# Kernel tuning notes

Measured on AMD Instinct MI355X. Metric: run time of the kernel, lower is better.

The kernel has to match this reference:

```python
import jax, jax.numpy as jnp
import numpy as np

F = 128          # num_features
NRBF = 20        # num_rbf_features
N_NODES = 25000
N_EDGES = 400000


def setup_inputs() -> dict:
    key = jax.random.key(0)
    ks = jax.random.split(key, 12)
    inp = {
        "idx_i": jax.random.randint(ks[0], (N_EDGES,), 0, N_NODES, dtype=jnp.int32),
        "idx_j": jax.random.randint(ks[1], (N_EDGES,), 0, N_NODES, dtype=jnp.int32),
        "rel_dir": jax.random.normal(ks[2], (N_EDGES, 3), dtype=jnp.float32),
        "rel_dist_cut": jax.random.uniform(ks[3], (N_EDGES,), dtype=jnp.float32),
        "rbf_features": jax.random.normal(ks[4], (N_EDGES, NRBF), dtype=jnp.float32),
        "scalar_features": jax.random.normal(ks[5], (N_NODES, F), dtype=jnp.float32),
        "vector_features": jax.random.normal(ks[6], (N_NODES, F, 3), dtype=jnp.float32),
        # scalar_network: Linear(F,F) -> SiLU -> Linear(F,3F)
        "W1": jax.random.normal(ks[7], (F, F), dtype=jnp.float32) / np.sqrt(F),
        "b1": jnp.zeros((F,), dtype=jnp.float32),
        "W2": jax.random.normal(ks[8], (3 * F, F), dtype=jnp.float32) / np.sqrt(F),
        "b2": jnp.zeros((3 * F,), dtype=jnp.float32),
        # rbf_network: Linear(NRBF, 3F)
        "Wr": jax.random.normal(ks[9], (3 * F, NRBF), dtype=jnp.float32) / np.sqrt(NRBF),
        "br": jnp.zeros((3 * F,), dtype=jnp.float32),
    }
    return inp


def reference(idx_i, idx_j, rel_dir, rel_dist_cut, rbf_features,
              scalar_features, vector_features, W1, b1, W2, b2, Wr, br):
    n_nodes = scalar_features.shape[0]
    # phi: per-node MLP -> [N, 3F]
    h = jax.nn.silu(scalar_features @ W1.T + b1)
    phi = h @ W2.T + b2
    # W: RBF-derived edge weights gated by cosine-cut distance -> [E, 3F]
    W = (rbf_features @ Wr.T + br) * rel_dist_cut[:, None]
    phi_W = phi[idx_j] * W                                  # [E, 3F]
    phi_W_vv, phi_W_ss, phi_W_vs = jnp.split(phi_W, 3, axis=-1)
    # scatter-add scalar residuals
    scalar_res = jax.ops.segment_sum(phi_W_ss, idx_i, num_segments=n_nodes)
    # per-edge vector messages [E, F, 3]
    vec_per_edge = (vector_features[idx_j] * phi_W_vv[..., None]
                    + phi_W_vs[..., None] * rel_dir[:, None, :])
    vector_res = jax.ops.segment_sum(vec_per_edge, idx_i, num_segments=n_nodes)
    return scalar_features + scalar_res, vector_features + vector_res
```

## Files before the change

### kernel.cpp

```cpp
#include <hip/hip_runtime.h>
#include <hip/hip_fp16.h>

#define F 128
#define F3 384
#define NRBF 20
#define NPB 16
#define CHUNK 64
#define PSN 32

typedef unsigned int u32;
typedef _Float16 half8 __attribute__((ext_vector_type(8)));
typedef float floatx4 __attribute__((ext_vector_type(4)));

__device__ __forceinline__ float2 uph(u32 u) {
    __half2 h = *(__half2*)&u;
    return __half22float2(h);
}
__device__ __forceinline__ u32 pkh(float a, float b) {
    __half2 h = __floats2half2_rn(a, b);
    return *(u32*)&h;
}

__device__ __forceinline__ float fdot2f(u32 a, u32 b, float c) {
#if defined(__has_builtin)
#if __has_builtin(__builtin_amdgcn_fdot2)
    typedef _Float16 h2 __attribute__((ext_vector_type(2)));
    return __builtin_amdgcn_fdot2(*(h2*)&a, *(h2*)&b, c, false);
#else
    float2 fa = uph(a), fb = uph(b);
    return fmaf(fa.x, fb.x, fmaf(fa.y, fb.y, c));
#endif
#else
    float2 fa = uph(a), fb = uph(b);
    return fmaf(fa.x, fb.x, fmaf(fa.y, fb.y, c));
#endif
}

__global__ void prep_kernel(const float* __restrict__ Wr,
                            const float* __restrict__ W1, const float* __restrict__ W2,
                            u32* __restrict__ WrTh, _Float16* __restrict__ Wh,
                            int* __restrict__ counts, int n_nodes) {
    int t = blockIdx.x * blockDim.x + threadIdx.x;
    if (t < 10 * F3) {
        int rr = t / F3, f = t % F3;
        WrTh[rr * F3 + f] = pkh(Wr[f * NRBF + 2 * rr], Wr[f * NRBF + 2 * rr + 1]);
        return;
    }
    int u = t - 10 * F3;
    if (u < (F + F3) * F) {
        int n = u >> 7, k = u & (F - 1);
        float w = (n < F) ? W1[n * F + k] : W2[(size_t)(n - F) * F + k];
        Wh[u] = (_Float16)w;
        return;
    }
    int z = u - (F + F3) * F;
    if (z < n_nodes) counts[z] = 0;
}

__global__ void hist_kernel(const int* __restrict__ idx_i, int* __restrict__ counts, int n_edges) {
    int e = blockIdx.x * blockDim.x + threadIdx.x;
    if (e < n_edges) atomicAdd(&counts[idx_i[e]], 1);
}

#define SCAN_T 1024
#define SCAN_MAXN 25600
__launch_bounds__(SCAN_T)
__global__ void scan_lds_kernel(const int* __restrict__ counts, int* __restrict__ row_start,
                                int* __restrict__ cursor, int n) {
    __shared__ int sbuf[SCAN_MAXN];
    __shared__ int partial[SCAN_T];
    int t = threadIdx.x;
    for (int i = t; i < n; i += SCAN_T) sbuf[i] = counts[i];
    __syncthreads();
    int C = (n + SCAN_T - 1) / SCAN_T;
    int beg = t * C, end = min(beg + C, n);
    int sum = 0;
    for (int i = beg; i < end; i++) sum += sbuf[i];
    partial[t] = sum;
    __syncthreads();
    for (int off = 1; off < SCAN_T; off <<= 1) {
        int v = (t >= off) ? partial[t - off] : 0;
        __syncthreads();
        partial[t] += v;
        __syncthreads();
    }
    int base = (t == 0) ? 0 : partial[t - 1];
    for (int i = beg; i < end; i++) { int c = sbuf[i]; sbuf[i] = base; base += c; }
    __syncthreads();
    for (int i = t; i < n; i += SCAN_T) { int v = sbuf[i]; row_start[i] = v; cursor[i] = v; }
    if (t == SCAN_T - 1) row_start[n] = partial[SCAN_T - 1];
}

__launch_bounds__(1024)
__global__ void scan_kernel(const int* __restrict__ counts, int* __restrict__ row_start,
                            int* __restrict__ cursor, int n) {
    __shared__ int partial[1024];
    int t = threadIdx.x;
    int C = (n + 1023) / 1024;
    int beg = t * C, end = min(beg + C, n);
    int sum = 0;
    for (int i = beg; i < end; i++) sum += counts[i];
    partial[t] = sum;
    __syncthreads();
    for (int off = 1; off < 1024; off <<= 1) {
        int v = (t >= off) ? partial[t - off] : 0;
        __syncthreads();
        partial[t] += v;
        __syncthreads();
    }
    int base = (t == 0) ? 0 : partial[t - 1];
    for (int i = beg; i < end; i++) {
        int c = counts[i];
        row_start[i] = base; cursor[i] = base; base += c;
    }
    if (t == 1023) row_start[n] = partial[1023];
}

__global__ void build_records(const int* __restrict__ idx_i, const int* __restrict__ idx_j,
                              const float* __restrict__ rel_dir, const float* __restrict__ rdc,
                              const float* __restrict__ rbf, int* __restrict__ cursor,
                              u32* __restrict__ recs, int n_edges) {
    int e = blockIdx.x * blockDim.x + threadIdx.x;
    if (e >= n_edges) return;
    int p = atomicAdd(&cursor[idx_i[e]], 1);
    u32 r[16];
    r[0] = (u32)idx_j[e];
    r[1] = __float_as_uint(rdc[e]);
    r[2] = __float_as_uint(rel_dir[e * 3 + 0]);
    r[3] = __float_as_uint(rel_dir[e * 3 + 1]);
    r[4] = __float_as_uint(rel_dir[e * 3 + 2]);
    const float* rb = rbf + (size_t)e * NRBF;
#pragma unroll
    for (int t = 0; t < 10; t++) r[5 + t] = pkh(rb[2 * t], rb[2 * t + 1]);
    r[15] = 0;
    float4* dst = (float4*)(recs + (size_t)p * 16);
    const float4* src = (const float4*)r;
    dst[0] = src[0]; dst[1] = src[1]; dst[2] = src[2]; dst[3] = src[3];
}

__global__ void scatter_kernel(const int* __restrict__ idx_i, int* __restrict__ cursor,
                               int* __restrict__ edge_order, int n_edges) {
    int e = blockIdx.x * blockDim.x + threadIdx.x;
    if (e < n_edges) {
        int p = atomicAdd(&cursor[idx_i[e]], 1);
        edge_order[p] = e;
    }
}

__launch_bounds__(128)
__global__ void phi_stage_kernel(const float* __restrict__ sf,
                                 const _Float16* __restrict__ Wh,
                                 const float* __restrict__ b1, const float* __restrict__ b2,
                                 const float* __restrict__ vf, __half* __restrict__ gbufh,
                                 int n_nodes) {
    __shared__ __align__(16) _Float16 stage[PSN * 768];
    _Float16 (*hl)[16][136] = reinterpret_cast<_Float16 (*)[16][136]>(stage);

    int tid = threadIdx.x;
    int lane = tid & 63;
    int wv = tid >> 6;
    int col = lane & 15;
    int kg = lane >> 4;
    int base = blockIdx.x * PSN;
    int row0 = base + wv * 16;

    half8 a1[4];
#pragma unroll
    for (int kb = 0; kb < 4; kb++) {
        int rr = row0 + col;
        if (rr >= n_nodes) rr = n_nodes - 1;
        const float4* xp = (const float4*)(sf + (size_t)rr * F + kb * 32 + kg * 8);
        float4 x0 = xp[0], x1 = xp[1];
        half8 a;
        a[0] = (_Float16)x0.x; a[1] = (_Float16)x0.y; a[2] = (_Float16)x0.z; a[3] = (_Float16)x0.w;
        a[4] = (_Float16)x1.x; a[5] = (_Float16)x1.y; a[6] = (_Float16)x1.z; a[7] = (_Float16)x1.w;
        a1[kb] = a;
    }

    floatx4 acc[8];
#pragma unroll
    for (int nt = 0; nt < 8; nt++) acc[nt] = (floatx4){0.f, 0.f, 0.f, 0.f};
#pragma unroll
    for (int nt = 0; nt < 8; nt++) {
#pragma unroll
        for (int kb = 0; kb < 4; kb++) {
            half8 b = *(const half8*)(Wh + (size_t)(nt * 16 + col) * F + kb * 32 + kg * 8);
            acc[nt] = __builtin_amdgcn_mfma_f32_16x16x32_f16(a1[kb], b, acc[nt], 0, 0, 0);
        }
    }
#pragma unroll
    for (int nt = 0; nt < 8; nt++) {
        int f1 = nt * 16 + col;
        float bb = b1[f1];
#pragma unroll
        for (int r = 0; r < 4; r++) {
            float v = acc[nt][r] + bb;
            float s = v / (1.f + __expf(-v));
            hl[wv][kg * 4 + r][f1] = (_Float16)s;
        }
    }
    __syncthreads();

    half8 a2[4];
#pragma unroll
    for (int kb = 0; kb < 4; kb++)
        a2[kb] = *(const half8*)&hl[wv][col][kb * 32 + kg * 8];
    __syncthreads();

#pragma unroll
    for (int c = 0; c < 3; c++) {
#pragma unroll
        for (int nt = 0; nt < 8; nt++) acc[nt] = (floatx4){0.f, 0.f, 0.f, 0.f};
#pragma unroll
        for (int nt = 0; nt < 8; nt++) {
#pragma unroll
            for (int kb = 0; kb < 4; kb++) {
                half8 b = *(const half8*)(Wh + (size_t)(F + c * 128 + nt * 16 + col) * F + kb * 32 + kg * 8);
                acc[nt] = __builtin_amdgcn_mfma_f32_16x16x32_f16(a2[kb], b, acc[nt], 0, 0, 0);
            }
        }
#pragma unroll
        for (int nt = 0; nt < 8; nt++) {
            int f2 = c * 128 + nt * 16 + col;
            float bb = b2[f2];
            int slot = (f2 & 63) * 12 + ((f2 >> 6) & 1) * 6 + (f2 >> 7);
#pragma unroll
            for (int r = 0; r < 4; r++) {
                int nl = wv * 16 + kg * 4 + r;
                stage[nl * 768 + slot] = (_Float16)(acc[nt][r] + bb);
            }
        }
    }

    for (int idx = tid; idx < PSN * 64; idx += 128) {
        int nl = idx >> 6, ln = idx & 63;
        int node = base + nl;
        if (node < n_nodes) {
            const float* v = vf + (size_t)node * F3;
            _Float16* s = stage + nl * 768 + ln * 12;
            s[3]  = (_Float16)v[ln * 3 + 0];
            s[4]  = (_Float16)v[ln * 3 + 1];
            s[5]  = (_Float16)v[ln * 3 + 2];
            s[9]  = (_Float16)v[(ln + 64) * 3 + 0];
            s[10] = (_Float16)v[(ln + 64) * 3 + 1];
            s[11] = (_Float16)v[(ln + 64) * 3 + 2];
        }
    }
    __syncthreads();

    const uint4* s4 = (const uint4*)stage;
    uint4* g4 = (uint4*)gbufh + (size_t)base * 96;
    for (int t = tid; t < PSN * 96; t += 128) {
        int node = base + t / 96;
        if (node < n_nodes) g4[t] = s4[t];
    }
}

__launch_bounds__(256)
__global__ void gather5_kernel(const float* __restrict__ sf, const float* __restrict__ vf,
                               const u32* __restrict__ WrTh, const float* __restrict__ br,
                               const u32* __restrict__ gbuf, const u32* __restrict__ recs,
                               const int* __restrict__ row_start,
                               float* __restrict__ out_s, float* __restrict__ out_v,
                               int n_nodes) {
    __shared__ u32 lsm[4][CHUNK * 16];
    int tid = threadIdx.x;
    int lane = tid & 63;
    int wvid = tid >> 6;
    int w = wvid & 1;
    int node = blockIdx.x * 2 + (wvid >> 1);
    if (node >= n_nodes) return;
    u32* lds = lsm[wvid];

    int fb = lane + 64 * w;
    u32 wrpk[3][10];
    float brv[3];
#pragma unroll
    for (int k = 0; k < 3; k++) {
        brv[k] = br[fb + 128 * k];
#pragma unroll
        for (int rr = 0; rr < 10; rr++)
            wrpk[k][rr] = WrTh[rr * F3 + fb + 128 * k];
    }

    float acc_s = 0.f, av0 = 0.f, av1 = 0.f, av2 = 0.f;
    int beg = row_start[node];
    int end = row_start[node + 1];

    for (int cb = beg; cb < end; cb += CHUNK) {
        int cnt = min(CHUNK, end - cb);
        {
            const float4* src = (const float4*)(recs + (size_t)cb * 16);
            int nf4 = cnt * 4;
            for (int t = lane; t < nf4; t += 64)
                ((float4*)lds)[t] = src[t];
        }

        auto issueL = [&](u32& g0, u32& g1, u32& g2, int m) {
            if (m < cnt) {
                int j = (int)lds[m * 16];
                const u32* gp = gbuf + (size_t)j * 384 + lane * 6 + w * 3;
                g0 = gp[0]; g1 = gp[1]; g2 = gp[2];
            }
        };
        auto computeE = [&](u32 g0, u32 g1, u32 g2, int m) {
            const uint4* q = (const uint4*)(lds + m * 16);
            uint4 q0 = q[0], q1 = q[1], q2 = q[2], q3 = q[3];
            float rd = __uint_as_float(q0.y);
            float dx = __uint_as_float(q0.z);
            float dy = __uint_as_float(q0.w);
            float dz = __uint_as_float(q1.x);
            u32 rbu[10] = { q1.y, q1.z, q1.w, q2.x, q2.y, q2.z, q2.w, q3.x, q3.y, q3.z };
            float W0 = brv[0], W1f = brv[1], W2f = brv[2];
#pragma unroll
            for (int rr = 0; rr < 10; rr++) {
                W0  = fdot2f(rbu[rr], wrpk[0][rr], W0);
                W1f = fdot2f(rbu[rr], wrpk[1][rr], W1f);
                W2f = fdot2f(rbu[rr], wrpk[2][rr], W2f);
            }
            float2 p01  = uph(g0);
            float2 p2v0 = uph(g1);
            float2 v12  = uph(g2);
            float pw0 = W0  * rd * p01.x;
            float pw1 = W1f * rd * p01.y;
            float pw2 = W2f * rd * p2v0.x;
            acc_s += pw1;
            av0 += p2v0.y * pw0 + pw2 * dx;
            av1 += v12.x  * pw0 + pw2 * dy;
            av2 += v12.y  * pw0 + pw2 * dz;
        };

        u32 A0, A1, A2, B0, B1, B2, C0, C1, C2, D0, D1, D2;
        issueL(A0, A1, A2, 0); issueL(B0, B1, B2, 1);
        issueL(C0, C1, C2, 2); issueL(D0, D1, D2, 3);
        int m = 0;
        while (true) {
            if (m >= cnt) break; computeE(A0, A1, A2, m); m++; issueL(A0, A1, A2, m + 3);
            if (m >= cnt) break; computeE(B0, B1, B2, m); m++; issueL(B0, B1, B2, m + 3);
            if (m >= cnt) break; computeE(C0, C1, C2, m); m++; issueL(C0, C1, C2, m + 3);
            if (m >= cnt) break; computeE(D0, D1, D2, m); m++; issueL(D0, D1, D2, m + 3);
        }
    }

    out_s[(size_t)node * F + fb] = sf[(size_t)node * F + fb] + acc_s;
    const float* vfi = vf + (size_t)node * F3 + fb * 3;
    float* ovi = out_v + (size_t)node * F3 + fb * 3;
    ovi[0] = vfi[0] + av0;
    ovi[1] = vfi[1] + av1;
    ovi[2] = vfi[2] + av2;
}

__launch_bounds__(256)
__global__ void gather3_kernel(const int* __restrict__ idx_j,
                               const float* __restrict__ rel_dir, const float* __restrict__ rdc,
                               const float* __restrict__ rbf,
                               const float* __restrict__ sf, const float* __restrict__ vf,
                               const u32* __restrict__ WrTh, const float* __restrict__ br,
                               const u32* __restrict__ gbuf,
                               const int* __restrict__ row_start, const int* __restrict__ edge_order,
                               float* __restrict__ out_s, float* __restrict__ out_v,
                               int n_nodes) {
    int lane = threadIdx.x & 63;
    int w = (threadIdx.x >> 6) & 1;
    int node = blockIdx.x * 2 + (threadIdx.x >> 7);
    if (node >= n_nodes) return;

    int fb = lane + 64 * w;
    u32 wrpk[3][10];
    float brv[3];
#pragma unroll
    for (int k = 0; k < 3; k++) {
        brv[k] = br[fb + 128 * k];
#pragma unroll
        for (int rr = 0; rr < 10; rr++)
            wrpk[k][rr] = WrTh[rr * F3 + fb + 128 * k];
    }

    float acc_s = 0.f, av0 = 0.f, av1 = 0.f, av2 = 0.f;
    int beg = row_start[node];
    int end = row_start[node + 1];

    for (int cb = beg; cb < end; cb += 64) {
        int cnt = min(64, end - cb);
        int jv = 0; float rdv = 0.f, dxv = 0.f, dyv = 0.f, dzv = 0.f;
        u32 rbm[10];
#pragma unroll
        for (int rr = 0; rr < 10; rr++) rbm[rr] = 0;
        if (lane < cnt) {
            int e = edge_order[cb + lane];
            jv = idx_j[e];
            rdv = rdc[e];
            dxv = rel_dir[e * 3 + 0]; dyv = rel_dir[e * 3 + 1]; dzv = rel_dir[e * 3 + 2];
            const float4* rp = (const float4*)(rbf + (size_t)e * NRBF);
            float4 r0 = rp[0], r1 = rp[1], r2 = rp[2], r3 = rp[3], r4 = rp[4];
            rbm[0] = pkh(r0.x, r0.y); rbm[1] = pkh(r0.z, r0.w);
            rbm[2] = pkh(r1.x, r1.y); rbm[3] = pkh(r1.z, r1.w);
            rbm[4] = pkh(r2.x, r2.y); rbm[5] = pkh(r2.z, r2.w);
            rbm[6] = pkh(r3.x, r3.y); rbm[7] = pkh(r3.z, r3.w);
            rbm[8] = pkh(r4.x, r4.y); rbm[9] = pkh(r4.z, r4.w);
        }
        auto issue = [&](u32& g0, u32& g1, u32& g2, int k) {
            int j = __shfl(jv, k, 64);
            const u32* gp = gbuf + (size_t)j * 384 + lane * 6 + w * 3;
            g0 = gp[0]; g1 = gp[1]; g2 = gp[2];
        };
        auto compute = [&](u32 g0, u32 g1, u32 g2, int k) {
            float rd = __shfl(rdv, k, 64);
            float dx = __shfl(dxv, k, 64);
            float dy = __shfl(dyv, k, 64);
            float dz = __shfl(dzv, k, 64);
            float W0 = brv[0], W1f = brv[1], W2f = brv[2];
#pragma unroll
            for (int rr = 0; rr < 10; rr++) {
                u32 rbi = (u32)__shfl((int)rbm[rr], k, 64);
                W0  = fdot2f(rbi, wrpk[0][rr], W0);
                W1f = fdot2f(rbi, wrpk[1][rr], W1f);
                W2f = fdot2f(rbi, wrpk[2][rr], W2f);
            }
            float2 p01 = uph(g0);
            float2 p2v0 = uph(g1);
            float2 v12 = uph(g2);
            float pw0 = W0 * rd * p01.x;
            float pw1 = W1f * rd * p01.y;
            float pw2 = W2f * rd * p2v0.x;
            acc_s += pw1;
            av0 += p2v0.y * pw0 + pw2 * dx;
            av1 += v12.x  * pw0 + pw2 * dy;
            av2 += v12.y  * pw0 + pw2 * dz;
        };
        u32 A0, A1, A2, B0, B1, B2;
        issue(A0, A1, A2, 0);
        int k = 0;
        while (k + 2 <= cnt) {
            issue(B0, B1, B2, k + 1);
            compute(A0, A1, A2, k);
            if (k + 2 < cnt) issue(A0, A1, A2, k + 2);
            compute(B0, B1, B2, k + 1);
            k += 2;
        }
        if (k < cnt) compute(A0, A1, A2, k);
    }

    out_s[(size_t)node * F + fb] = sf[(size_t)node * F + fb] + acc_s;
    const float* vfi = vf + (size_t)node * F3 + fb * 3;
    float* ovi = out_v + (size_t)node * F3 + fb * 3;
    ovi[0] = vfi[0] + av0;
    ovi[1] = vfi[1] + av1;
    ovi[2] = vfi[2] + av2;
}

__global__ void transpose_wr(const float* __restrict__ Wr, float* __restrict__ WrT) {
    int idx = blockIdx.x * blockDim.x + threadIdx.x;
    if (idx < F3 * NRBF) {
        int f = idx / NRBF, r = idx % NRBF;
        WrT[r * F3 + f] = Wr[idx];
    }
}

__global__ void init_out(const float* __restrict__ sf, const float* __restrict__ vf,
                         float* __restrict__ out, int n_scalar, int n_total) {
    int i = blockIdx.x * blockDim.x + threadIdx.x;
    int n4 = n_total >> 2;
    if (i < n4) {
        float4 v;
        int base = i << 2;
        if (base < n_scalar) v = ((const float4*)sf)[i];
        else                 v = ((const float4*)vf)[i - (n_scalar >> 2)];
        ((float4*)out)[i] = v;
    }
}

__launch_bounds__(256)
__global__ void phi32_kernel(const float* __restrict__ sf,
                             const float* __restrict__ W1, const float* __restrict__ b1,
                             const float* __restrict__ W2, const float* __restrict__ b2,
                             float* __restrict__ phi, int n_nodes) {
    __shared__ float xs[NPB][F];
    __shared__ float hs[NPB][F];
    int tid = threadIdx.x;
    int nb = blockIdx.x * NPB;
    for (int t = tid; t < NPB * F / 4; t += 256) {
        int n  = t / (F / 4);
        int k4 = t % (F / 4);
        float4 v = make_float4(0.f, 0.f, 0.f, 0.f);
        if (nb + n < n_nodes) v = ((const float4*)(sf + (size_t)(nb + n) * F))[k4];
        ((float4*)&xs[n][0])[k4] = v;
    }
    __syncthreads();
    {
        int f = tid & (F - 1);
        int half_ = tid >> 7;
        float acc[8];
#pragma unroll
        for (int nn = 0; nn < 8; nn++) acc[nn] = 0.f;
        const float* w1row = W1 + (size_t)f * F;
        for (int k = 0; k < F; k++) {
            float w = w1row[k];
#pragma unroll
            for (int nn = 0; nn < 8; nn++)
                acc[nn] += xs[half_ * 8 + nn][k] * w;
        }
        float b = b1[f];
#pragma unroll
        for (int nn = 0; nn < 8; nn++) {
            float v = acc[nn] + b;
            hs[half_ * 8 + nn][f] = v / (1.f + __expf(-v));
        }
    }
    __syncthreads();
    for (int f = tid; f < F3; f += 256) {
        float acc[NPB];
#pragma unroll
        for (int n = 0; n < NPB; n++) acc[n] = 0.f;
        const float* w2row = W2 + (size_t)f * F;
        for (int k = 0; k < F; k++) {
            float w = w2row[k];
#pragma unroll
            for (int n = 0; n < NPB; n++)
                acc[n] += hs[n][k] * w;
        }
        float b = b2[f];
        for (int n = 0; n < NPB; n++)
            if (nb + n < n_nodes)
                phi[(size_t)(nb + n) * F3 + f] = acc[n] + b;
    }
}

__launch_bounds__(256)
__global__ void edge_kernel(const int* __restrict__ idx_i, const int* __restrict__ idx_j,
                            const float* __restrict__ rel_dir, const float* __restrict__ rdc,
                            const float* __restrict__ rbf,
                            const float* __restrict__ vf,
                            const float* __restrict__ WrT, const float* __restrict__ br,
                            const float* __restrict__ phi,
                            float* __restrict__ out_s, float* __restrict__ out_v,
                            int n_edges) {
    int lane = threadIdx.x & 63;
    int e = (int)((blockIdx.x * (unsigned)blockDim.x + threadIdx.x) >> 6);
    if (e >= n_edges) return;
    int i = idx_i[e], j = idx_j[e];
    float rd = rdc[e];
    float d0 = rel_dir[e * 3 + 0], d1 = rel_dir[e * 3 + 1], d2 = rel_dir[e * 3 + 2];
    float rb[NRBF];
#pragma unroll
    for (int r = 0; r < NRBF; r++) rb[r] = rbf[(size_t)e * NRBF + r];
    const float* pj = phi + (size_t)j * F3;
    float pw[6];
#pragma unroll
    for (int q = 0; q < 6; q++) {
        int f = lane + 64 * q;
        float acc = br[f];
#pragma unroll
        for (int r = 0; r < NRBF; r++)
            acc += rb[r] * WrT[r * F3 + f];
        pw[q] = acc * rd * pj[f];
    }
    atomicAdd(&out_s[(size_t)i * F + lane],       pw[2]);
    atomicAdd(&out_s[(size_t)i * F + lane + 64],  pw[3]);
    const float* vfj = vf + (size_t)j * F * 3;
    float* ovi = out_v + (size_t)i * F * 3;
#pragma unroll
    for (int h = 0; h < 2; h++) {
        int f = lane + 64 * h;
        float vv = pw[h];
        float vs = pw[4 + h];
        atomicAdd(&ovi[f * 3 + 0], vfj[f * 3 + 0] * vv + vs * d0);
        atomicAdd(&ovi[f * 3 + 1], vfj[f * 3 + 1] * vv + vs * d1);
        atomicAdd(&ovi[f * 3 + 2], vfj[f * 3 + 2] * vv + vs * d2);
    }
}

extern "C" void kernel_launch(void* const* d_in, const int* in_sizes, int n_in,
                              void* d_out, int out_size, void* d_ws, size_t ws_size,
                              hipStream_t stream) {
    const int*   idx_i   = (const int*)d_in[0];
    const int*   idx_j   = (const int*)d_in[1];
    const float* rel_dir = (const float*)d_in[2];
    const float* rdc     = (const float*)d_in[3];
    const float* rbf     = (const float*)d_in[4];
    const float* sf      = (const float*)d_in[5];
    const float* vf      = (const float*)d_in[6];
    const float* W1      = (const float*)d_in[7];
    const float* b1      = (const float*)d_in[8];
    const float* W2      = (const float*)d_in[9];
    const float* b2      = (const float*)d_in[10];
    const float* Wr      = (const float*)d_in[11];
    const float* br      = (const float*)d_in[12];

    int E = in_sizes[0];
    int N = in_sizes[5] / F;

    float* out_s = (float*)d_out;
    float* out_v = out_s + (size_t)N * F;

    size_t off = 0;
    auto slab = [&](size_t bytes) { size_t o = off; off = (off + bytes + 255) & ~(size_t)255; return o; };
    size_t o_wrth = slab((size_t)10 * F3 * sizeof(u32));
    size_t o_wh   = slab((size_t)(F + F3) * F * sizeof(_Float16));
    size_t o_gbuf = slab((size_t)N * 768 * sizeof(__half));
    size_t o_cnt  = slab((size_t)N * sizeof(int));
    size_t o_row  = slab((size_t)(N + 1) * sizeof(int));
    size_t o_rec  = slab((size_t)E * 64);
    size_t need_v5 = off;

    size_t off3 = 0;
    auto slab3 = [&](size_t bytes) { size_t o = off3; off3 = (off3 + bytes + 255) & ~(size_t)255; return o; };
    size_t t_wrth = slab3((size_t)10 * F3 * sizeof(u32));
    size_t t_wh   = slab3((size_t)(F + F3) * F * sizeof(_Float16));
    size_t t_gbuf = slab3((size_t)N * 768 * sizeof(__half));
    size_t t_cnt  = slab3((size_t)N * sizeof(int));
    size_t t_row  = slab3((size_t)(N + 1) * sizeof(int));
    size_t t_ord  = slab3((size_t)E * sizeof(int));
    size_t need_v3 = off3;

    int prep_threads = 10 * F3 + (F + F3) * F + N;
    int HB = (E + 255) / 256;
    int PSB = (N + PSN - 1) / PSN;

    if (ws_size >= need_v5) {
        u32*      WrTh      = (u32*)((char*)d_ws + o_wrth);
        _Float16* Wh        = (_Float16*)((char*)d_ws + o_wh);
        __half*   gbufh     = (__half*)((char*)d_ws + o_gbuf);
        u32*      gbuf      = (u32*)gbufh;
        int*      counts    = (int*)((char*)d_ws + o_cnt);
        int*      cursor    = counts;
        int*      row_start = (int*)((char*)d_ws + o_row);
        u32*      recs      = (u32*)((char*)d_ws + o_rec);

        prep_kernel<<<(prep_threads + 255) / 256, 256, 0, stream>>>(Wr, W1, W2, WrTh, Wh, counts, N);
        hist_kernel<<<HB, 256, 0, stream>>>(idx_i, counts, E);
        if (N <= SCAN_MAXN)
            scan_lds_kernel<<<1, SCAN_T, 0, stream>>>(counts, row_start, cursor, N);
        else
            scan_kernel<<<1, 1024, 0, stream>>>(counts, row_start, cursor, N);
        build_records<<<HB, 256, 0, stream>>>(idx_i, idx_j, rel_dir, rdc, rbf, cursor, recs, E);
        phi_stage_kernel<<<PSB, 128, 0, stream>>>(sf, Wh, b1, b2, vf, gbufh, N);
        gather5_kernel<<<(N + 1) / 2, 256, 0, stream>>>(sf, vf, WrTh, br, gbuf, recs,
                                                        row_start, out_s, out_v, N);
    } else if (ws_size >= need_v3) {
        u32*      WrTh      = (u32*)((char*)d_ws + t_wrth);
        _Float16* Wh        = (_Float16*)((char*)d_ws + t_wh);
        __half*   gbufh     = (__half*)((char*)d_ws + t_gbuf);
        u32*      gbuf      = (u32*)gbufh;
        int*      counts    = (int*)((char*)d_ws + t_cnt);
        int*      cursor    = counts;
        int*      row_start = (int*)((char*)d_ws + t_row);
        int*      edge_ord  = (int*)((char*)d_ws + t_ord);

        prep_kernel<<<(prep_threads + 255) / 256, 256, 0, stream>>>(Wr, W1, W2, WrTh, Wh, counts, N);
        hist_kernel<<<HB, 256, 0, stream>>>(idx_i, counts, E);
        if (N <= SCAN_MAXN)
            scan_lds_kernel<<<1, SCAN_T, 0, stream>>>(counts, row_start, cursor, N);
        else
            scan_kernel<<<1, 1024, 0, stream>>>(counts, row_start, cursor, N);
        phi_stage_kernel<<<PSB, 128, 0, stream>>>(sf, Wh, b1, b2, vf, gbufh, N);
        scatter_kernel<<<HB, 256, 0, stream>>>(idx_i, cursor, edge_ord, E);
        gather3_kernel<<<(N + 1) / 2, 256, 0, stream>>>(idx_j, rel_dir, rdc, rbf, sf, vf,
                                                        WrTh, br, gbuf, row_start, edge_ord,
                                                        out_s, out_v, N);
    } else {
        size_t off2 = 0;
        auto slab2 = [&](size_t bytes) { size_t o = off2; off2 = (off2 + bytes + 255) & ~(size_t)255; return o; };
        size_t f_wrt = slab2((size_t)F3 * NRBF * sizeof(float));
        size_t f_phi = slab2((size_t)N * F3 * sizeof(float));
        float* WrT = (float*)((char*)d_ws + f_wrt);
        float* phi = (float*)((char*)d_ws + f_phi);

        int n_scalar = N * F;
        int n_total  = N * F * 4;
        init_out<<<(n_total / 4 + 255) / 256, 256, 0, stream>>>(sf, vf, (float*)d_out, n_scalar, n_total);
        transpose_wr<<<(F3 * NRBF + 255) / 256, 256, 0, stream>>>(Wr, WrT);
        phi32_kernel<<<(N + NPB - 1) / NPB, 256, 0, stream>>>(sf, W1, b1, W2, b2, phi, N);
        edge_kernel<<<(E + 3) / 4, 256, 0, stream>>>(idx_i, idx_j, rel_dir, rdc, rbf,
                                                     vf, WrT, br, phi, out_s, out_v, E);
    }
}
```

Baseline: 220.9 us.

## Replace materialized edge records with edge-order indices and fuse histogram into prep

Stops writing sorted 64-byte per-edge records to global memory. A scatter kernel now writes only a sorted edge-order index, and the gather kernel builds each record in LDS on the fly with indirect loads of idx_j, rel_dir, rdc and rbf. The histogram is merged into the weight-pack kernel as extra blocks, and the counts reset becomes a memset. This saves a large global write and read of records, but the gather now does scattered, uncoalesced per-edge loads.

```diff
diff --git a/kernel.cpp b/kernel.cpp
--- a/kernel.cpp
+++ b/kernel.cpp
@@ -36,11 +36,18 @@
 #endif
 }
 
-__global__ void prep_kernel(const float* __restrict__ Wr,
-                            const float* __restrict__ W1, const float* __restrict__ W2,
-                            u32* __restrict__ WrTh, _Float16* __restrict__ Wh,
-                            int* __restrict__ counts, int n_nodes) {
-    int t = blockIdx.x * blockDim.x + threadIdx.x;
+__global__ void prep2_kernel(const float* __restrict__ Wr,
+                             const float* __restrict__ W1, const float* __restrict__ W2,
+                             u32* __restrict__ WrTh, _Float16* __restrict__ Wh,
+                             const int* __restrict__ idx_i, int* __restrict__ counts,
+                             int n_edges, int PKB) {
+    int blk = blockIdx.x, tid = threadIdx.x;
+    if (blk >= PKB) {
+        int e = (blk - PKB) * 256 + tid;
+        if (e < n_edges) atomicAdd(&counts[idx_i[e]], 1);
+        return;
+    }
+    int t = blk * 256 + tid;
     if (t < 10 * F3) {
         int rr = t / F3, f = t % F3;
         WrTh[rr * F3 + f] = pkh(Wr[f * NRBF + 2 * rr], Wr[f * NRBF + 2 * rr + 1]);
@@ -51,15 +58,7 @@
         int n = u >> 7, k = u & (F - 1);
         float w = (n < F) ? W1[n * F + k] : W2[(size_t)(n - F) * F + k];
         Wh[u] = (_Float16)w;
-        return;
-    }
-    int z = u - (F + F3) * F;
-    if (z < n_nodes) counts[z] = 0;
-}
-
-__global__ void hist_kernel(const int* __restrict__ idx_i, int* __restrict__ counts, int n_edges) {
-    int e = blockIdx.x * blockDim.x + threadIdx.x;
-    if (e < n_edges) atomicAdd(&counts[idx_i[e]], 1);
+    }
 }
 
 #define SCAN_T 1024
@@ -114,28 +113,6 @@
         row_start[i] = base; cursor[i] = base; base += c;
     }
     if (t == 1023) row_start[n] = partial[1023];
-}
-
-__global__ void build_records(const int* __restrict__ idx_i, const int* __restrict__ idx_j,
-                              const float* __restrict__ rel_dir, const float* __restrict__ rdc,
-                              const float* __restrict__ rbf, int* __restrict__ cursor,
-                              u32* __restrict__ recs, int n_edges) {
-    int e = blockIdx.x * blockDim.x + threadIdx.x;
-    if (e >= n_edges) return;
-    int p = atomicAdd(&cursor[idx_i[e]], 1);
-    u32 r[16];
-    r[0] = (u32)idx_j[e];
-    r[1] = __float_as_uint(rdc[e]);
-    r[2] = __float_as_uint(rel_dir[e * 3 + 0]);
-    r[3] = __float_as_uint(rel_dir[e * 3 + 1]);
-    r[4] = __float_as_uint(rel_dir[e * 3 + 2]);
-    const float* rb = rbf + (size_t)e * NRBF;
-#pragma unroll
-    for (int t = 0; t < 10; t++) r[5 + t] = pkh(rb[2 * t], rb[2 * t + 1]);
-    r[15] = 0;
-    float4* dst = (float4*)(recs + (size_t)p * 16);
-    const float4* src = (const float4*)r;
-    dst[0] = src[0]; dst[1] = src[1]; dst[2] = src[2]; dst[3] = src[3];
 }
 
 __global__ void scatter_kernel(const int* __restrict__ idx_i, int* __restrict__ cursor,
@@ -257,10 +234,13 @@
 }
 
 __launch_bounds__(256)
-__global__ void gather5_kernel(const float* __restrict__ sf, const float* __restrict__ vf,
+__global__ void gather7_kernel(const int* __restrict__ idx_j,
+                               const float* __restrict__ rel_dir, const float* __restrict__ rdc,
+                               const float* __restrict__ rbf,
+                               const float* __restrict__ sf, const float* __restrict__ vf,
                                const u32* __restrict__ WrTh, const float* __restrict__ br,
-                               const u32* __restrict__ gbuf, const u32* __restrict__ recs,
-                               const int* __restrict__ row_start,
+                               const u32* __restrict__ gbuf,
+                               const int* __restrict__ row_start, const int* __restrict__ edge_order,
                                float* __restrict__ out_s, float* __restrict__ out_v,
                                int n_nodes) {
     __shared__ u32 lsm[4][CHUNK * 16];
@@ -289,11 +269,19 @@
 
     for (int cb = beg; cb < end; cb += CHUNK) {
         int cnt = min(CHUNK, end - cb);
-        {
-            const float4* src = (const float4*)(recs + (size_t)cb * 16);
-            int nf4 = cnt * 4;
-            for (int t = lane; t < nf4; t += 64)
-                ((float4*)lds)[t] = src[t];
+
+        if (lane < cnt) {
+            int e = edge_order[cb + lane];
+            int j = idx_j[e];
+            float rd = rdc[e];
+            float d0 = rel_dir[e * 3 + 0], d1 = rel_dir[e * 3 + 1], d2 = rel_dir[e * 3 + 2];
+            const float4* rp = (const float4*)(rbf + (size_t)e * NRBF);
+            float4 r0 = rp[0], r1 = rp[1], r2 = rp[2], r3 = rp[3], r4 = rp[4];
+            uint4* rec = (uint4*)(lds + lane * 16);
+            rec[0] = make_uint4((u32)j, __float_as_uint(rd), __float_as_uint(d0), __float_as_uint(d1));
+            rec[1] = make_uint4(__float_as_uint(d2), pkh(r0.x, r0.y), pkh(r0.z, r0.w), pkh(r1.x, r1.y));
+            rec[2] = make_uint4(pkh(r1.z, r1.w), pkh(r2.x, r2.y), pkh(r2.z, r2.w), pkh(r3.x, r3.y));
+            rec[3] = make_uint4(pkh(r3.z, r3.w), pkh(r4.x, r4.y), pkh(r4.z, r4.w), 0u);
         }
 
         auto issueL = [&](u32& g0, u32& g1, u32& g2, int m) {
@@ -350,105 +338,6 @@
     ovi[2] = vfi[2] + av2;
 }
 
-__launch_bounds__(256)
-__global__ void gather3_kernel(const int* __restrict__ idx_j,
-                               const float* __restrict__ rel_dir, const float* __restrict__ rdc,
-                               const float* __restrict__ rbf,
-                               const float* __restrict__ sf, const float* __restrict__ vf,
-                               const u32* __restrict__ WrTh, const float* __restrict__ br,
-                               const u32* __restrict__ gbuf,
-                               const int* __restrict__ row_start, const int* __restrict__ edge_order,
-                               float* __restrict__ out_s, float* __restrict__ out_v,
-                               int n_nodes) {
-    int lane = threadIdx.x & 63;
-    int w = (threadIdx.x >> 6) & 1;
-    int node = blockIdx.x * 2 + (threadIdx.x >> 7);
-    if (node >= n_nodes) return;
-
-    int fb = lane + 64 * w;
-    u32 wrpk[3][10];
-    float brv[3];
-#pragma unroll
-    for (int k = 0; k < 3; k++) {
-        brv[k] = br[fb + 128 * k];
-#pragma unroll
-        for (int rr = 0; rr < 10; rr++)
-            wrpk[k][rr] = WrTh[rr * F3 + fb + 128 * k];
-    }
-
-    float acc_s = 0.f, av0 = 0.f, av1 = 0.f, av2 = 0.f;
-    int beg = row_start[node];
-    int end = row_start[node + 1];
-
-    for (int cb = beg; cb < end; cb += 64) {
-        int cnt = min(64, end - cb);
-        int jv = 0; float rdv = 0.f, dxv = 0.f, dyv = 0.f, dzv = 0.f;
-        u32 rbm[10];
-#pragma unroll
-        for (int rr = 0; rr < 10; rr++) rbm[rr] = 0;
-        if (lane < cnt) {
-            int e = edge_order[cb + lane];
-            jv = idx_j[e];
-            rdv = rdc[e];
-            dxv = rel_dir[e * 3 + 0]; dyv = rel_dir[e * 3 + 1]; dzv = rel_dir[e * 3 + 2];
-            const float4* rp = (const float4*)(rbf + (size_t)e * NRBF);
-            float4 r0 = rp[0], r1 = rp[1], r2 = rp[2], r3 = rp[3], r4 = rp[4];
-            rbm[0] = pkh(r0.x, r0.y); rbm[1] = pkh(r0.z, r0.w);
-            rbm[2] = pkh(r1.x, r1.y); rbm[3] = pkh(r1.z, r1.w);
-            rbm[4] = pkh(r2.x, r2.y); rbm[5] = pkh(r2.z, r2.w);
-            rbm[6] = pkh(r3.x, r3.y); rbm[7] = pkh(r3.z, r3.w);
-            rbm[8] = pkh(r4.x, r4.y); rbm[9] = pkh(r4.z, r4.w);
-        }
-        auto issue = [&](u32& g0, u32& g1, u32& g2, int k) {
-            int j = __shfl(jv, k, 64);
-            const u32* gp = gbuf + (size_t)j * 384 + lane * 6 + w * 3;
-            g0 = gp[0]; g1 = gp[1]; g2 = gp[2];
-        };
-        auto compute = [&](u32 g0, u32 g1, u32 g2, int k) {
-            float rd = __shfl(rdv, k, 64);
-            float dx = __shfl(dxv, k, 64);
-            float dy = __shfl(dyv, k, 64);
-            float dz = __shfl(dzv, k, 64);
-            float W0 = brv[0], W1f = brv[1], W2f = brv[2];
-#pragma unroll
-            for (int rr = 0; rr < 10; rr++) {
-                u32 rbi = (u32)__shfl((int)rbm[rr], k, 64);
-                W0  = fdot2f(rbi, wrpk[0][rr], W0);
-                W1f = fdot2f(rbi, wrpk[1][rr], W1f);
-                W2f = fdot2f(rbi, wrpk[2][rr], W2f);
-            }
-            float2 p01 = uph(g0);
-            float2 p2v0 = uph(g1);
-            float2 v12 = uph(g2);
-            float pw0 = W0 * rd * p01.x;
-            float pw1 = W1f * rd * p01.y;
-            float pw2 = W2f * rd * p2v0.x;
-            acc_s += pw1;
-            av0 += p2v0.y * pw0 + pw2 * dx;
-            av1 += v12.x  * pw0 + pw2 * dy;
-            av2 += v12.y  * pw0 + pw2 * dz;
-        };
-        u32 A0, A1, A2, B0, B1, B2;
-        issue(A0, A1, A2, 0);
-        int k = 0;
-        while (k + 2 <= cnt) {
-            issue(B0, B1, B2, k + 1);
-            compute(A0, A1, A2, k);
-            if (k + 2 < cnt) issue(A0, A1, A2, k + 2);
-            compute(B0, B1, B2, k + 1);
-            k += 2;
-        }
-        if (k < cnt) compute(A0, A1, A2, k);
-    }
-
-    out_s[(size_t)node * F + fb] = sf[(size_t)node * F + fb] + acc_s;
-    const float* vfi = vf + (size_t)node * F3 + fb * 3;
-    float* ovi = out_v + (size_t)node * F3 + fb * 3;
-    ovi[0] = vfi[0] + av0;
-    ovi[1] = vfi[1] + av1;
-    ovi[2] = vfi[2] + av2;
-}
-
 __global__ void transpose_wr(const float* __restrict__ Wr, float* __restrict__ WrT) {
     int idx = blockIdx.x * blockDim.x + threadIdx.x;
     if (idx < F3 * NRBF) {
@@ -600,24 +489,15 @@
     size_t o_gbuf = slab((size_t)N * 768 * sizeof(__half));
     size_t o_cnt  = slab((size_t)N * sizeof(int));
     size_t o_row  = slab((size_t)(N + 1) * sizeof(int));
-    size_t o_rec  = slab((size_t)E * 64);
-    size_t need_v5 = off;
-
-    size_t off3 = 0;
-    auto slab3 = [&](size_t bytes) { size_t o = off3; off3 = (off3 + bytes + 255) & ~(size_t)255; return o; };
-    size_t t_wrth = slab3((size_t)10 * F3 * sizeof(u32));
-    size_t t_wh   = slab3((size_t)(F + F3) * F * sizeof(_Float16));
-    size_t t_gbuf = slab3((size_t)N * 768 * sizeof(__half));
-    size_t t_cnt  = slab3((size_t)N * sizeof(int));
-    size_t t_row  = slab3((size_t)(N + 1) * sizeof(int));
-    size_t t_ord  = slab3((size_t)E * sizeof(int));
-    size_t need_v3 = off3;
-
-    int prep_threads = 10 * F3 + (F + F3) * F + N;
-    int HB = (E + 255) / 256;
+    size_t o_ord  = slab((size_t)E * sizeof(int));
+    size_t need_v7 = off;
+
+    int pack_threads = 10 * F3 + (F + F3) * F;
+    int PKB = (pack_threads + 255) / 256;
+    int HB  = (E + 255) / 256;
     int PSB = (N + PSN - 1) / PSN;
 
-    if (ws_size >= need_v5) {
+    if (ws_size >= need_v7) {
         u32*      WrTh      = (u32*)((char*)d_ws + o_wrth);
         _Float16* Wh        = (_Float16*)((char*)d_ws + o_wh);
         __half*   gbufh     = (__half*)((char*)d_ws + o_gbuf);
@@ -625,37 +505,17 @@
         int*      counts    = (int*)((char*)d_ws + o_cnt);
         int*      cursor    = counts;
         int*      row_start = (int*)((char*)d_ws + o_row);
-        u32*      recs      = (u32*)((char*)d_ws + o_rec);
-
-        prep_kernel<<<(prep_threads + 255) / 256, 256, 0, stream>>>(Wr, W1, W2, WrTh, Wh, counts, N);
-        hist_kernel<<<HB, 256, 0, stream>>>(idx_i, counts, E);
+        int*      edge_ord  = (int*)((char*)d_ws + o_ord);
+
+        hipMemsetAsync(counts, 0, (size_t)N * sizeof(int), stream);
+        prep2_kernel<<<PKB + HB, 256, 0, stream>>>(Wr, W1, W2, WrTh, Wh, idx_i, counts, E, PKB);
         if (N <= SCAN_MAXN)
             scan_lds_kernel<<<1, SCAN_T, 0, stream>>>(counts, row_start, cursor, N);
         else
             scan_kernel<<<1, 1024, 0, stream>>>(counts, row_start, cursor, N);
-        build_records<<<HB, 256, 0, stream>>>(idx_i, idx_j, rel_dir, rdc, rbf, cursor, recs, E);
+        scatter_kernel<<<HB, 256, 0, stream>>>(idx_i, cursor, edge_ord, E);
         phi_stage_kernel<<<PSB, 128, 0, stream>>>(sf, Wh, b1, b2, vf, gbufh, N);
-        gather5_kernel<<<(N + 1) / 2, 256, 0, stream>>>(sf, vf, WrTh, br, gbuf, recs,
-                                                        row_start, out_s, out_v, N);
-    } else if (ws_size >= need_v3) {
-        u32*      WrTh      = (u32*)((char*)d_ws + t_wrth);
-        _Float16* Wh        = (_Float16*)((char*)d_ws + t_wh);
-        __half*   gbufh     = (__half*)((char*)d_ws + t_gbuf);
-        u32*      gbuf      = (u32*)gbufh;
-        int*      counts    = (int*)((char*)d_ws + t_cnt);
-        int*      cursor    = counts;
-        int*      row_start = (int*)((char*)d_ws + t_row);
-        int*      edge_ord  = (int*)((char*)d_ws + t_ord);
-
-        prep_kernel<<<(prep_threads + 255) / 256, 256, 0, stream>>>(Wr, W1, W2, WrTh, Wh, counts, N);
-        hist_kernel<<<HB, 256, 0, stream>>>(idx_i, counts, E);
-        if (N <= SCAN_MAXN)
-            scan_lds_kernel<<<1, SCAN_T, 0, stream>>>(counts, row_start, cursor, N);
-        else
-            scan_kernel<<<1, 1024, 0, stream>>>(counts, row_start, cursor, N);
-        phi_stage_kernel<<<PSB, 128, 0, stream>>>(sf, Wh, b1, b2, vf, gbufh, N);
-        scatter_kernel<<<HB, 256, 0, stream>>>(idx_i, cursor, edge_ord, E);
-        gather3_kernel<<<(N + 1) / 2, 256, 0, stream>>>(idx_j, rel_dir, rdc, rbf, sf, vf,
+        gather7_kernel<<<(N + 1) / 2, 256, 0, stream>>>(idx_j, rel_dir, rdc, rbf, sf, vf,
                                                         WrTh, br, gbuf, row_start, edge_ord,
                                                         out_s, out_v, N);
     } else {
```

Result: slower. 240.6 us (+8.9%).
